# Kernel tuning notes

Hardware: AMD Instinct MI355X
Metric: run time of the kernel (lower is better)

Reference implementation:

```python
import jax, jax.numpy as jnp
import numpy as np

N = 100000   # nodes
E = 640000   # edges
D = 128      # in_channels
C = 40       # out_channels (classes)


def setup_inputs() -> dict:
    key = jax.random.key(0)
    ks = jax.random.split(key, 6)
    x = jax.random.normal(ks[0], (N, D), jnp.float32)
    edge_index = jax.random.randint(ks[1], (2, E), 0, N)
    edge_weight = jax.random.uniform(ks[2], (E,), jnp.float32)
    # 8 block convs (4 blocks x 2) stacked, + final conv
    Wb = jax.random.normal(ks[3], (8, D, D), jnp.float32) / np.sqrt(D)
    bb = jnp.zeros((8, D), jnp.float32)
    Wf = jax.random.normal(ks[4], (D, C), jnp.float32) / np.sqrt(D)
    bf = jnp.zeros((C,), jnp.float32)
    return dict(x=x, edge_index=edge_index, edge_weight=edge_weight,
                Wb=Wb, bb=bb, Wf=Wf, bf=bf)


def _gcn(x, W, b, src, dst, w):
    """PyG GCNConv (normalize=True) with self-loops already appended to src/dst/w."""
    n = x.shape[0]
    h = x @ W                                   # [N, out]
    deg = jax.ops.segment_sum(w, dst, num_segments=n)
    dinv = jnp.where(deg > 0, jax.lax.rsqrt(deg), 0.0)
    norm = dinv[src] * w * dinv[dst]            # [E+N]
    out = jax.ops.segment_sum(h[src] * norm[:, None], dst, num_segments=n)
    return out + b


def reference(x, edge_index, edge_weight, Wb, bb, Wf, bf):
    n = x.shape[0]
    loop = jnp.arange(n)
    src = jnp.concatenate([edge_index[0], loop])
    dst = jnp.concatenate([edge_index[1], loop])
    w = jnp.concatenate([edge_weight, jnp.ones((n,), x.dtype)])
    # forward only runs blocks 1-4 (blocks 5-7 unused in the original forward)
    for i in range(4):
        identity = x
        x = jax.nn.relu(_gcn(x, Wb[2 * i], bb[2 * i], src, dst, w))
        # dropout: identity in eval mode
        x = jax.nn.relu(_gcn(x, Wb[2 * i + 1], bb[2 * i + 1], src, dst, w))
        # F.normalize: row-wise L2 with eps=1e-12
        x = x / jnp.maximum(jnp.linalg.norm(x, axis=1, keepdims=True), 1e-12)
        x = (x + identity) / 2
    x = _gcn(x, Wf, bf, src, dst, w)
    return jax.nn.log_softmax(x, axis=1)
```

## Files before the change

### kernel.cpp

```cpp
#include <hip/hip_runtime.h>
#include <math.h>

#define NN 100000
#define EE 640000
#define DD 128
#define CC 40
#define FIXS 4194304.0f

typedef __bf16 bf16x8 __attribute__((ext_vector_type(8)));
typedef float f32x4 __attribute__((ext_vector_type(4)));
typedef unsigned short us8 __attribute__((ext_vector_type(8)));

__device__ inline unsigned short f2b(float f) {
    union { float f; unsigned u; } v; v.f = f;
    unsigned u = v.u;
    return (unsigned short)((u + 0x7FFFu + ((u >> 16) & 1u)) >> 16);
}
__device__ inline float b2f(unsigned short b) {
    union { unsigned u; float f; } v; v.u = ((unsigned)b) << 16;
    return v.f;
}


__global__ __launch_bounds__(256) void k_edge1(const int* __restrict__ dst,
                                               const float* __restrict__ w,
                                               unsigned long long* __restrict__ degcnt,
                                               int* __restrict__ pos) {
    int e = blockIdx.x * 256 + threadIdx.x;
    if (e < EE) {
        int d = dst[e];
        unsigned long long pk =
            ((unsigned long long)(unsigned)(w[e] * FIXS) << 32) | 1ull;
        unsigned long long old = atomicAdd(&degcnt[d], pk);
        pos[e] = (int)(old & 0xffffffffull);
    }
}

__global__ __launch_bounds__(256) void k_scan1(const unsigned long long* __restrict__ degcnt,
                                               float* __restrict__ dinv,
                                               int* __restrict__ out,
                                               int* __restrict__ partial) {
    __shared__ int lds[256];
    int t = threadIdx.x;
    int base = blockIdx.x * 1024 + t * 4;
    int v[4]; int s = 0;
    #pragma unroll
    for (int j = 0; j < 4; ++j) {
        int idx = base + j;
        unsigned long long dc = (idx < NN) ? degcnt[idx] : 0ull;
        v[j] = (int)(dc & 0xffffffffull);
        s += v[j];
        if (idx < NN)
            dinv[idx] = rsqrtf((float)(unsigned)(dc >> 32) * (1.0f / FIXS) + 1.0f);
    }
    lds[t] = s;
    __syncthreads();
    for (int off = 1; off < 256; off <<= 1) {
        int x = lds[t];
        int y = (t >= off) ? lds[t - off] : 0;
        __syncthreads();
        lds[t] = x + y;
        __syncthreads();
    }
    int excl = lds[t] - s;
    if (t == 255) partial[blockIdx.x] = lds[255];
    int run = excl;
    #pragma unroll
    for (int j = 0; j < 4; ++j) {
        int idx = base + j;
        if (idx < NN) out[idx] = run;
        run += v[j];
    }
}

__global__ __launch_bounds__(128) void k_scan2(int* __restrict__ partial) {
    __shared__ int lds[128];
    int t = threadIdx.x;
    int v = (t < 98) ? partial[t] : 0;
    lds[t] = v;
    __syncthreads();
    for (int off = 1; off < 128; off <<= 1) {
        int x = lds[t];
        int y = (t >= off) ? lds[t - off] : 0;
        __syncthreads();
        lds[t] = x + y;
        __syncthreads();
    }
    if (t < 98) partial[t] = lds[t] - v;
}

__global__ __launch_bounds__(256) void k_scan3(int* __restrict__ rp,
                                               const int* __restrict__ partial) {
    int i = blockIdx.x * 256 + threadIdx.x;
    if (i < NN) rp[i] += partial[i >> 10];
    if (i == 0) rp[NN] = EE;
}

__global__ __launch_bounds__(256) void k_scatter(const int* __restrict__ src,
                                                 const int* __restrict__ dst,
                                                 const float* __restrict__ w,
                                                 const float* __restrict__ dinv,
                                                 const int* __restrict__ rp,
                                                 const int* __restrict__ pos,
                                                 int* __restrict__ col,
                                                 float* __restrict__ val) {
    int e = blockIdx.x * 256 + threadIdx.x;
    if (e < EE) {
        int s = src[e], d = dst[e];
        int p = rp[d] + pos[e];
        col[p] = s;
        val[p] = dinv[s] * w[e] * dinv[d];
    }
}


__global__ __launch_bounds__(256) void k_prep_w(const float* __restrict__ Wb,
                                                unsigned short* __restrict__ WT) {
    int idx = blockIdx.x * 256 + threadIdx.x;
    if (idx >= 8 * DD * DD) return;
    int m = idx >> 14;
    int n = (idx >> 7) & 127;
    int k = idx & 127;
    WT[idx] = f2b(Wb[(size_t)m * DD * DD + (size_t)k * DD + n]);
}

__global__ __launch_bounds__(256) void k_prep_wf(const float* __restrict__ Wf,
                                                 unsigned short* __restrict__ WfT) {
    int idx = blockIdx.x * 256 + threadIdx.x;
    if (idx >= 48 * DD) return;
    int n = idx >> 7;
    int k = idx & 127;
    WfT[idx] = (n < CC) ? f2b(Wf[(size_t)k * CC + n]) : 0;
}

__global__ __launch_bounds__(256) void k_x2bf(const float* __restrict__ x,
                                              float* __restrict__ A,
                                              unsigned short* __restrict__ Abf) {
    int idx = blockIdx.x * 256 + threadIdx.x;
    if (idx >= NN * DD / 4) return;
    float4 v = ((const float4*)x)[idx];
    ((float4*)A)[idx] = v;
    ushort4 r;
    r.x = f2b(v.x); r.y = f2b(v.y); r.z = f2b(v.z); r.w = f2b(v.w);
    ((ushort4*)Abf)[idx] = r;
}

__global__ __launch_bounds__(256) void k_mm_mfma(const unsigned short* __restrict__ X,
                                                 const unsigned short* __restrict__ WT,
                                                 unsigned short* __restrict__ H) {
    int wid = threadIdx.x >> 6;
    int lane = threadIdx.x & 63;
    int r0 = blockIdx.x * 64 + wid * 16;
    int sl = lane & 15, g = lane >> 4;
    int arow = r0 + sl;
    if (arow >= NN) arow = NN - 1;

    f32x4 acc[8];
    #pragma unroll
    for (int n = 0; n < 8; ++n) acc[n] = (f32x4){0.f, 0.f, 0.f, 0.f};

    const bf16x8* xrow = (const bf16x8*)(X + (size_t)arow * DD);
    #pragma unroll
    for (int kc = 0; kc < 4; ++kc) {
        bf16x8 a = xrow[kc * 4 + g];
        #pragma unroll
        for (int n = 0; n < 8; ++n) {
            const bf16x8* wrow = (const bf16x8*)(WT + (size_t)(n * 16 + sl) * DD);
            bf16x8 b = wrow[kc * 4 + g];
            acc[n] = __builtin_amdgcn_mfma_f32_16x16x32_bf16(a, b, acc[n], 0, 0, 0);
        }
    }
    #pragma unroll
    for (int n = 0; n < 8; ++n) {
        #pragma unroll
        for (int v = 0; v < 4; ++v) {
            int row = r0 + g * 4 + v;
            if (row < NN) H[(size_t)row * DD + n * 16 + sl] = f2b(acc[n][v]);
        }
    }
}

__global__ __launch_bounds__(256) void k_mm_final(const unsigned short* __restrict__ X,
                                                  const unsigned short* __restrict__ WfT,
                                                  const float* __restrict__ bf_,
                                                  float* __restrict__ out) {
    int wid = threadIdx.x >> 6;
    int lane = threadIdx.x & 63;
    int r0 = blockIdx.x * 64 + wid * 16;
    int sl = lane & 15, g = lane >> 4;
    int arow = r0 + sl;
    if (arow >= NN) arow = NN - 1;

    f32x4 acc[3];
    #pragma unroll
    for (int n = 0; n < 3; ++n) acc[n] = (f32x4){0.f, 0.f, 0.f, 0.f};

    const bf16x8* xrow = (const bf16x8*)(X + (size_t)arow * DD);
    #pragma unroll
    for (int kc = 0; kc < 4; ++kc) {
        bf16x8 a = xrow[kc * 4 + g];
        #pragma unroll
        for (int n = 0; n < 3; ++n) {
            const bf16x8* wrow = (const bf16x8*)(WfT + (size_t)(n * 16 + sl) * DD);
            bf16x8 b = wrow[kc * 4 + g];
            acc[n] = __builtin_amdgcn_mfma_f32_16x16x32_bf16(a, b, acc[n], 0, 0, 0);
        }
    }
    #pragma unroll
    for (int v = 0; v < 4; ++v) {
        int row = r0 + g * 4 + v;
        float vv[3];
        #pragma unroll
        for (int n = 0; n < 3; ++n) {
            int c = n * 16 + sl;
            vv[n] = (c < CC) ? acc[n][v] + bf_[c] : -3.0e38f;
        }
        float m = fmaxf(fmaxf(vv[0], vv[1]), vv[2]);
        m = fmaxf(m, __shfl_xor(m, 1));
        m = fmaxf(m, __shfl_xor(m, 2));
        m = fmaxf(m, __shfl_xor(m, 4));
        m = fmaxf(m, __shfl_xor(m, 8));
        float s = 0.f;
        #pragma unroll
        for (int n = 0; n < 3; ++n)
            s += (n * 16 + sl < CC) ? expf(vv[n] - m) : 0.f;
        s += __shfl_xor(s, 1);
        s += __shfl_xor(s, 2);
        s += __shfl_xor(s, 4);
        s += __shfl_xor(s, 8);
        float ls = logf(s);
        #pragma unroll
        for (int n = 0; n < 3; ++n) {
            int c = n * 16 + sl;
            if (row < NN && c < CC) out[(size_t)row * CC + c] = vv[n] - m - ls;
        }
    }
}


#define AGG_CORE(h_, node_, sl_, a_)                                        \
    {                                                                       \
        float dv = dinv[node_];                                             \
        float dv2 = dv * dv;                                                \
        us8 m_ = ((const us8*)(h_ + (size_t)node_ * DD))[sl_];              \
        _Pragma("unroll")                                                   \
        for (int j = 0; j < 8; ++j) a_[j] = dv2 * b2f(m_[j]);               \
        int e = rp[node_], end = rp[node_ + 1];                             \
        for (; e + 4 <= end; e += 4) {                                      \
            int s0 = col[e], s1 = col[e + 1], s2 = col[e + 2], s3 = col[e + 3]; \
            float v0 = val[e], v1 = val[e + 1], v2 = val[e + 2], v3 = val[e + 3]; \
            us8 q0 = ((const us8*)(h_ + (size_t)s0 * DD))[sl_];             \
            us8 q1 = ((const us8*)(h_ + (size_t)s1 * DD))[sl_];             \
            us8 q2 = ((const us8*)(h_ + (size_t)s2 * DD))[sl_];             \
            us8 q3 = ((const us8*)(h_ + (size_t)s3 * DD))[sl_];             \
            _Pragma("unroll")                                               \
            for (int j = 0; j < 8; ++j)                                     \
                a_[j] += (v0 * b2f(q0[j]) + v1 * b2f(q1[j]))                \
                       + (v2 * b2f(q2[j]) + v3 * b2f(q3[j]));               \
        }                                                                   \
        for (; e < end; ++e) {                                              \
            int s0 = col[e];                                                \
            float v0 = val[e];                                              \
            us8 q0 = ((const us8*)(h_ + (size_t)s0 * DD))[sl_];             \
            _Pragma("unroll")                                               \
            for (int j = 0; j < 8; ++j) a_[j] += v0 * b2f(q0[j]);           \
        }                                                                   \
    }

__global__ __launch_bounds__(256) void k_agg128(const unsigned short* __restrict__ h,
                                                const float* __restrict__ dinv,
                                                const int* __restrict__ rp,
                                                const int* __restrict__ col,
                                                const float* __restrict__ val,
                                                const float* __restrict__ bias,
                                                unsigned short* __restrict__ outb) {
    int node = blockIdx.x * 16 + (threadIdx.x >> 4);
    int sl = threadIdx.x & 15;
    if (node >= NN) return;
    float a[8];
    AGG_CORE(h, node, sl, a);
    float4 bz0 = ((const float4*)bias)[sl * 2];
    float4 bz1 = ((const float4*)bias)[sl * 2 + 1];
    float bb[8] = {bz0.x, bz0.y, bz0.z, bz0.w, bz1.x, bz1.y, bz1.z, bz1.w};
    us8 r;
    #pragma unroll
    for (int j = 0; j < 8; ++j) r[j] = f2b(fmaxf(a[j] + bb[j], 0.f));
    ((us8*)(outb + (size_t)node * DD))[sl] = r;
}

__global__ __launch_bounds__(256) void k_agg128_nr(const unsigned short* __restrict__ h,
                                                   const float* __restrict__ dinv,
                                                   const int* __restrict__ rp,
                                                   const int* __restrict__ col,
                                                   const float* __restrict__ val,
                                                   const float* __restrict__ bias,
                                                   float* __restrict__ A,
                                                   unsigned short* __restrict__ Abf) {
    int node = blockIdx.x * 16 + (threadIdx.x >> 4);
    int sl = threadIdx.x & 15;
    if (node >= NN) return;
    float a[8];
    AGG_CORE(h, node, sl, a);
    float4 bz0 = ((const float4*)bias)[sl * 2];
    float4 bz1 = ((const float4*)bias)[sl * 2 + 1];
    float bb[8] = {bz0.x, bz0.y, bz0.z, bz0.w, bz1.x, bz1.y, bz1.z, bz1.w};
    float ss = 0.f;
    #pragma unroll
    for (int j = 0; j < 8; ++j) {
        a[j] = fmaxf(a[j] + bb[j], 0.f);
        ss += a[j] * a[j];
    }
    ss += __shfl_xor(ss, 1);
    ss += __shfl_xor(ss, 2);
    ss += __shfl_xor(ss, 4);
    ss += __shfl_xor(ss, 8);
    float sc = 1.0f / fmaxf(sqrtf(ss), 1e-12f);
    float4 a0 = ((const float4*)(A + (size_t)node * DD))[sl * 2];
    float4 a1 = ((const float4*)(A + (size_t)node * DD))[sl * 2 + 1];
    float av[8] = {a0.x, a0.y, a0.z, a0.w, a1.x, a1.y, a1.z, a1.w};
    us8 rb;
    #pragma unroll
    for (int j = 0; j < 8; ++j) {
        av[j] = (a[j] * sc + av[j]) * 0.5f;
        rb[j] = f2b(av[j]);
    }
    float4 o0 = {av[0], av[1], av[2], av[3]};
    float4 o1 = {av[4], av[5], av[6], av[7]};
    ((float4*)(A + (size_t)node * DD))[sl * 2] = o0;
    ((float4*)(A + (size_t)node * DD))[sl * 2 + 1] = o1;
    ((us8*)(Abf + (size_t)node * DD))[sl] = rb;
}

__global__ __launch_bounds__(256) void k_agg_plain(const unsigned short* __restrict__ h,
                                                   const float* __restrict__ dinv,
                                                   const int* __restrict__ rp,
                                                   const int* __restrict__ col,
                                                   const float* __restrict__ val,
                                                   unsigned short* __restrict__ outb) {
    int node = blockIdx.x * 16 + (threadIdx.x >> 4);
    int sl = threadIdx.x & 15;
    if (node >= NN) return;
    float a[8];
    AGG_CORE(h, node, sl, a);
    us8 r;
    #pragma unroll
    for (int j = 0; j < 8; ++j) r[j] = f2b(a[j]);
    ((us8*)(outb + (size_t)node * DD))[sl] = r;
}


extern "C" void kernel_launch(void* const* d_in, const int* in_sizes, int n_in,
                              void* d_out, int out_size, void* d_ws, size_t ws_size,
                              hipStream_t stream) {
    const float* x  = (const float*)d_in[0];
    const int*   ei = (const int*)d_in[1];
    const float* ew = (const float*)d_in[2];
    const float* Wb = (const float*)d_in[3];
    const float* bb = (const float*)d_in[4];
    const float* Wf = (const float*)d_in[5];
    const float* bf_ = (const float*)d_in[6];
    const int* src = ei;
    const int* dst = ei + EE;
    float* out = (float*)d_out;

    char* p = (char*)d_ws;
    float*              A      = (float*)p;              p += (size_t)NN * DD * 4;
    unsigned short*     Abf    = (unsigned short*)p;     p += (size_t)NN * DD * 2;
    unsigned short*     Bbf    = (unsigned short*)p;     p += (size_t)NN * DD * 2;
    unsigned short*     Cbf    = (unsigned short*)p;     p += (size_t)NN * DD * 2;
    unsigned short*     Gbf    = (unsigned short*)p;     p += (size_t)NN * DD * 2;
    unsigned short*     WT     = (unsigned short*)p;     p += (size_t)8 * DD * DD * 2;
    unsigned short*     WfT    = (unsigned short*)p;     p += (size_t)48 * DD * 2;
    unsigned long long* degcnt = (unsigned long long*)p; p += (size_t)NN * 8;
    float* dinv = (float*)p; p += (size_t)NN * 4;
    int*   rp   = (int*)p;   p += (size_t)(NN + 1) * 4;
    int*   pos  = (int*)p;   p += (size_t)EE * 4;
    int*   col  = (int*)p;   p += (size_t)EE * 4;
    float* val  = (float*)p; p += (size_t)EE * 4;
    int*   partial = (int*)p; p += 128 * 4;

    hipMemsetAsync(degcnt, 0, (size_t)NN * 8, stream);

    k_edge1<<<(EE + 255) / 256, 256, 0, stream>>>(dst, ew, degcnt, pos);
    k_scan1<<<98, 256, 0, stream>>>(degcnt, dinv, rp, partial);
    k_scan2<<<1, 128, 0, stream>>>(partial);
    k_scan3<<<(NN + 255) / 256, 256, 0, stream>>>(rp, partial);
    k_scatter<<<(EE + 255) / 256, 256, 0, stream>>>(src, dst, ew, dinv, rp, pos, col, val);

    k_prep_w<<<(8 * DD * DD + 255) / 256, 256, 0, stream>>>(Wb, WT);
    k_prep_wf<<<(48 * DD + 255) / 256, 256, 0, stream>>>(Wf, WfT);
    k_x2bf<<<(NN * DD / 4 + 255) / 256, 256, 0, stream>>>(x, A, Abf);

    for (int blk = 0; blk < 4; ++blk) {
        k_mm_mfma<<<(NN + 63) / 64, 256, 0, stream>>>(Abf, WT + (size_t)(2 * blk) * DD * DD, Bbf);
        k_agg128<<<(NN + 15) / 16, 256, 0, stream>>>(Bbf, dinv, rp, col, val, bb + (size_t)(2 * blk) * DD, Cbf);
        k_mm_mfma<<<(NN + 63) / 64, 256, 0, stream>>>(Cbf, WT + (size_t)(2 * blk + 1) * DD * DD, Bbf);
        k_agg128_nr<<<(NN + 15) / 16, 256, 0, stream>>>(Bbf, dinv, rp, col, val, bb + (size_t)(2 * blk + 1) * DD, A, Abf);
    }
    k_agg_plain<<<(NN + 15) / 16, 256, 0, stream>>>(Abf, dinv, rp, col, val, Gbf);
    k_mm_final<<<(NN + 63) / 64, 256, 0, stream>>>(Gbf, WfT, bf_, out);
}
```

Baseline: 725.0 us.

## Reorder final GCN to matmul-then-aggregate and drop fp32 residual copy

The final layer now projects to 40 (padded to 64) classes before aggregation, so the last sparse gather reads 64-wide bf16 rows instead of 128-wide. Bias and log_softmax are fused into the new aggregation kernel. The fp32 residual buffer is removed, and the residual now comes from the bf16 activations. This cuts memory traffic but adds extra bf16 rounding on the residual path, which may affect accuracy.

```diff
diff --git a/kernel.cpp b/kernel.cpp
--- a/kernel.cpp
+++ b/kernel.cpp
@@ -127,19 +127,17 @@
 __global__ __launch_bounds__(256) void k_prep_wf(const float* __restrict__ Wf,
                                                  unsigned short* __restrict__ WfT) {
     int idx = blockIdx.x * 256 + threadIdx.x;
-    if (idx >= 48 * DD) return;
+    if (idx >= 64 * DD) return;
     int n = idx >> 7;
     int k = idx & 127;
     WfT[idx] = (n < CC) ? f2b(Wf[(size_t)k * CC + n]) : 0;
 }
 
 __global__ __launch_bounds__(256) void k_x2bf(const float* __restrict__ x,
-                                              float* __restrict__ A,
                                               unsigned short* __restrict__ Abf) {
     int idx = blockIdx.x * 256 + threadIdx.x;
     if (idx >= NN * DD / 4) return;
     float4 v = ((const float4*)x)[idx];
-    ((float4*)A)[idx] = v;
     ushort4 r;
     r.x = f2b(v.x); r.y = f2b(v.y); r.z = f2b(v.z); r.w = f2b(v.w);
     ((ushort4*)Abf)[idx] = r;
@@ -180,10 +178,9 @@
     }
 }
 
-__global__ __launch_bounds__(256) void k_mm_final(const unsigned short* __restrict__ X,
-                                                  const unsigned short* __restrict__ WfT,
-                                                  const float* __restrict__ bf_,
-                                                  float* __restrict__ out) {
+__global__ __launch_bounds__(256) void k_mm40b(const unsigned short* __restrict__ X,
+                                               const unsigned short* __restrict__ WfT,
+                                               unsigned short* __restrict__ H) {
     int wid = threadIdx.x >> 6;
     int lane = threadIdx.x & 63;
     int r0 = blockIdx.x * 64 + wid * 16;
@@ -191,68 +188,47 @@
     int arow = r0 + sl;
     if (arow >= NN) arow = NN - 1;
 
-    f32x4 acc[3];
-    #pragma unroll
-    for (int n = 0; n < 3; ++n) acc[n] = (f32x4){0.f, 0.f, 0.f, 0.f};
+    f32x4 acc[4];
+    #pragma unroll
+    for (int n = 0; n < 4; ++n) acc[n] = (f32x4){0.f, 0.f, 0.f, 0.f};
 
     const bf16x8* xrow = (const bf16x8*)(X + (size_t)arow * DD);
     #pragma unroll
     for (int kc = 0; kc < 4; ++kc) {
         bf16x8 a = xrow[kc * 4 + g];
         #pragma unroll
-        for (int n = 0; n < 3; ++n) {
+        for (int n = 0; n < 4; ++n) {
             const bf16x8* wrow = (const bf16x8*)(WfT + (size_t)(n * 16 + sl) * DD);
             bf16x8 b = wrow[kc * 4 + g];
             acc[n] = __builtin_amdgcn_mfma_f32_16x16x32_bf16(a, b, acc[n], 0, 0, 0);
         }
     }
     #pragma unroll
-    for (int v = 0; v < 4; ++v) {
-        int row = r0 + g * 4 + v;
-        float vv[3];
-        #pragma unroll
-        for (int n = 0; n < 3; ++n) {
-            int c = n * 16 + sl;
-            vv[n] = (c < CC) ? acc[n][v] + bf_[c] : -3.0e38f;
+    for (int n = 0; n < 4; ++n) {
+        #pragma unroll
+        for (int v = 0; v < 4; ++v) {
+            int row = r0 + g * 4 + v;
+            if (row < NN) H[(size_t)row * 64 + n * 16 + sl] = f2b(acc[n][v]);
         }
-        float m = fmaxf(fmaxf(vv[0], vv[1]), vv[2]);
-        m = fmaxf(m, __shfl_xor(m, 1));
-        m = fmaxf(m, __shfl_xor(m, 2));
-        m = fmaxf(m, __shfl_xor(m, 4));
-        m = fmaxf(m, __shfl_xor(m, 8));
-        float s = 0.f;
-        #pragma unroll
-        for (int n = 0; n < 3; ++n)
-            s += (n * 16 + sl < CC) ? expf(vv[n] - m) : 0.f;
-        s += __shfl_xor(s, 1);
-        s += __shfl_xor(s, 2);
-        s += __shfl_xor(s, 4);
-        s += __shfl_xor(s, 8);
-        float ls = logf(s);
-        #pragma unroll
-        for (int n = 0; n < 3; ++n) {
-            int c = n * 16 + sl;
-            if (row < NN && c < CC) out[(size_t)row * CC + c] = vv[n] - m - ls;
-        }
-    }
-}
-
-
-#define AGG_CORE(h_, node_, sl_, a_)                                        \
+    }
+}
+
+
+#define AGG_CORE(h_, node_, sl_, a_, STRIDE_)                               \
     {                                                                       \
         float dv = dinv[node_];                                             \
         float dv2 = dv * dv;                                                \
-        us8 m_ = ((const us8*)(h_ + (size_t)node_ * DD))[sl_];              \
+        us8 m_ = ((const us8*)(h_ + (size_t)node_ * STRIDE_))[sl_];         \
         _Pragma("unroll")                                                   \
         for (int j = 0; j < 8; ++j) a_[j] = dv2 * b2f(m_[j]);               \
         int e = rp[node_], end = rp[node_ + 1];                             \
         for (; e + 4 <= end; e += 4) {                                      \
             int s0 = col[e], s1 = col[e + 1], s2 = col[e + 2], s3 = col[e + 3]; \
             float v0 = val[e], v1 = val[e + 1], v2 = val[e + 2], v3 = val[e + 3]; \
-            us8 q0 = ((const us8*)(h_ + (size_t)s0 * DD))[sl_];             \
-            us8 q1 = ((const us8*)(h_ + (size_t)s1 * DD))[sl_];             \
-            us8 q2 = ((const us8*)(h_ + (size_t)s2 * DD))[sl_];             \
-            us8 q3 = ((const us8*)(h_ + (size_t)s3 * DD))[sl_];             \
+            us8 q0 = ((const us8*)(h_ + (size_t)s0 * STRIDE_))[sl_];        \
+            us8 q1 = ((const us8*)(h_ + (size_t)s1 * STRIDE_))[sl_];        \
+            us8 q2 = ((const us8*)(h_ + (size_t)s2 * STRIDE_))[sl_];        \
+            us8 q3 = ((const us8*)(h_ + (size_t)s3 * STRIDE_))[sl_];        \
             _Pragma("unroll")                                               \
             for (int j = 0; j < 8; ++j)                                     \
                 a_[j] += (v0 * b2f(q0[j]) + v1 * b2f(q1[j]))                \
@@ -261,7 +237,7 @@
         for (; e < end; ++e) {                                              \
             int s0 = col[e];                                                \
             float v0 = val[e];                                              \
-            us8 q0 = ((const us8*)(h_ + (size_t)s0 * DD))[sl_];             \
+            us8 q0 = ((const us8*)(h_ + (size_t)s0 * STRIDE_))[sl_];        \
             _Pragma("unroll")                                               \
             for (int j = 0; j < 8; ++j) a_[j] += v0 * b2f(q0[j]);           \
         }                                                                   \
@@ -278,7 +254,7 @@
     int sl = threadIdx.x & 15;
     if (node >= NN) return;
     float a[8];
-    AGG_CORE(h, node, sl, a);
+    AGG_CORE(h, node, sl, a, DD);
     float4 bz0 = ((const float4*)bias)[sl * 2];
     float4 bz1 = ((const float4*)bias)[sl * 2 + 1];
     float bb[8] = {bz0.x, bz0.y, bz0.z, bz0.w, bz1.x, bz1.y, bz1.z, bz1.w};
@@ -294,13 +270,12 @@
                                                    const int* __restrict__ col,
                                                    const float* __restrict__ val,
                                                    const float* __restrict__ bias,
-                                                   float* __restrict__ A,
                                                    unsigned short* __restrict__ Abf) {
     int node = blockIdx.x * 16 + (threadIdx.x >> 4);
     int sl = threadIdx.x & 15;
     if (node >= NN) return;
     float a[8];
-    AGG_CORE(h, node, sl, a);
+    AGG_CORE(h, node, sl, a, DD);
     float4 bz0 = ((const float4*)bias)[sl * 2];
     float4 bz1 = ((const float4*)bias)[sl * 2 + 1];
     float bb[8] = {bz0.x, bz0.y, bz0.z, bz0.w, bz1.x, bz1.y, bz1.z, bz1.w};
@@ -315,37 +290,60 @@
     ss += __shfl_xor(ss, 4);
     ss += __shfl_xor(ss, 8);
     float sc = 1.0f / fmaxf(sqrtf(ss), 1e-12f);
-    float4 a0 = ((const float4*)(A + (size_t)node * DD))[sl * 2];
-    float4 a1 = ((const float4*)(A + (size_t)node * DD))[sl * 2 + 1];
-    float av[8] = {a0.x, a0.y, a0.z, a0.w, a1.x, a1.y, a1.z, a1.w};
+    us8 oldb = ((const us8*)(Abf + (size_t)node * DD))[sl];
     us8 rb;
     #pragma unroll
-    for (int j = 0; j < 8; ++j) {
-        av[j] = (a[j] * sc + av[j]) * 0.5f;
-        rb[j] = f2b(av[j]);
-    }
-    float4 o0 = {av[0], av[1], av[2], av[3]};
-    float4 o1 = {av[4], av[5], av[6], av[7]};
-    ((float4*)(A + (size_t)node * DD))[sl * 2] = o0;
-    ((float4*)(A + (size_t)node * DD))[sl * 2 + 1] = o1;
+    for (int j = 0; j < 8; ++j)
+        rb[j] = f2b((a[j] * sc + b2f(oldb[j])) * 0.5f);
     ((us8*)(Abf + (size_t)node * DD))[sl] = rb;
 }
 
-__global__ __launch_bounds__(256) void k_agg_plain(const unsigned short* __restrict__ h,
+__global__ __launch_bounds__(256) void k_agg_final(const unsigned short* __restrict__ h,
                                                    const float* __restrict__ dinv,
                                                    const int* __restrict__ rp,
                                                    const int* __restrict__ col,
                                                    const float* __restrict__ val,
-                                                   unsigned short* __restrict__ outb) {
-    int node = blockIdx.x * 16 + (threadIdx.x >> 4);
-    int sl = threadIdx.x & 15;
+                                                   const float* __restrict__ bias,
+                                                   float* __restrict__ out) {
+    int node = blockIdx.x * 32 + (threadIdx.x >> 3);
+    int sl = threadIdx.x & 7;
     if (node >= NN) return;
     float a[8];
-    AGG_CORE(h, node, sl, a);
-    us8 r;
-    #pragma unroll
-    for (int j = 0; j < 8; ++j) r[j] = f2b(a[j]);
-    ((us8*)(outb + (size_t)node * DD))[sl] = r;
+    AGG_CORE(h, node, sl, a, 64);
+    bool real = sl < 5;
+    float vv[8];
+    if (real) {
+        float4 bz0 = ((const float4*)bias)[sl * 2];
+        float4 bz1 = ((const float4*)bias)[sl * 2 + 1];
+        float bb[8] = {bz0.x, bz0.y, bz0.z, bz0.w, bz1.x, bz1.y, bz1.z, bz1.w};
+        #pragma unroll
+        for (int j = 0; j < 8; ++j) vv[j] = a[j] + bb[j];
+    } else {
+        #pragma unroll
+        for (int j = 0; j < 8; ++j) vv[j] = -3.0e38f;
+    }
+    float m = vv[0];
+    #pragma unroll
+    for (int j = 1; j < 8; ++j) m = fmaxf(m, vv[j]);
+    m = fmaxf(m, __shfl_xor(m, 1));
+    m = fmaxf(m, __shfl_xor(m, 2));
+    m = fmaxf(m, __shfl_xor(m, 4));
+    float s = 0.f;
+    if (real) {
+        #pragma unroll
+        for (int j = 0; j < 8; ++j) s += expf(vv[j] - m);
+    }
+    s += __shfl_xor(s, 1);
+    s += __shfl_xor(s, 2);
+    s += __shfl_xor(s, 4);
+    float ls = m + logf(s);
+    if (real) {
+        float4 o0 = {vv[0] - ls, vv[1] - ls, vv[2] - ls, vv[3] - ls};
+        float4 o1 = {vv[4] - ls, vv[5] - ls, vv[6] - ls, vv[7] - ls};
+        float* orow = out + (size_t)node * CC + sl * 8;
+        *(float4*)(orow) = o0;
+        *(float4*)(orow + 4) = o1;
+    }
 }
 
 
@@ -364,13 +362,12 @@
     float* out = (float*)d_out;
 
     char* p = (char*)d_ws;
-    float*              A      = (float*)p;              p += (size_t)NN * DD * 4;
     unsigned short*     Abf    = (unsigned short*)p;     p += (size_t)NN * DD * 2;
     unsigned short*     Bbf    = (unsigned short*)p;     p += (size_t)NN * DD * 2;
     unsigned short*     Cbf    = (unsigned short*)p;     p += (size_t)NN * DD * 2;
-    unsigned short*     Gbf    = (unsigned short*)p;     p += (size_t)NN * DD * 2;
+    unsigned short*     H48    = (unsigned short*)p;     p += (size_t)NN * 64 * 2;
     unsigned short*     WT     = (unsigned short*)p;     p += (size_t)8 * DD * DD * 2;
-    unsigned short*     WfT    = (unsigned short*)p;     p += (size_t)48 * DD * 2;
+    unsigned short*     WfT    = (unsigned short*)p;     p += (size_t)64 * DD * 2;
     unsigned long long* degcnt = (unsigned long long*)p; p += (size_t)NN * 8;
     float* dinv = (float*)p; p += (size_t)NN * 4;
     int*   rp   = (int*)p;   p += (size_t)(NN + 1) * 4;
@@ -388,15 +385,15 @@
     k_scatter<<<(EE + 255) / 256, 256, 0, stream>>>(src, dst, ew, dinv, rp, pos, col, val);
 
     k_prep_w<<<(8 * DD * DD + 255) / 256, 256, 0, stream>>>(Wb, WT);
-    k_prep_wf<<<(48 * DD + 255) / 256, 256, 0, stream>>>(Wf, WfT);
-    k_x2bf<<<(NN * DD / 4 + 255) / 256, 256, 0, stream>>>(x, A, Abf);
+    k_prep_wf<<<(64 * DD + 255) / 256, 256, 0, stream>>>(Wf, WfT);
+    k_x2bf<<<(NN * DD / 4 + 255) / 256, 256, 0, stream>>>(x, Abf);
 
     for (int blk = 0; blk < 4; ++blk) {
         k_mm_mfma<<<(NN + 63) / 64, 256, 0, stream>>>(Abf, WT + (size_t)(2 * blk) * DD * DD, Bbf);
         k_agg128<<<(NN + 15) / 16, 256, 0, stream>>>(Bbf, dinv, rp, col, val, bb + (size_t)(2 * blk) * DD, Cbf);
         k_mm_mfma<<<(NN + 63) / 64, 256, 0, stream>>>(Cbf, WT + (size_t)(2 * blk + 1) * DD * DD, Bbf);
-        k_agg128_nr<<<(NN + 15) / 16, 256, 0, stream>>>(Bbf, dinv, rp, col, val, bb + (size_t)(2 * blk + 1) * DD, A, Abf);
-    }
-    k_agg_plain<<<(NN + 15) / 16, 256, 0, stream>>>(Abf, dinv, rp, col, val, Gbf);
-    k_mm_final<<<(NN + 63) / 64, 256, 0, stream>>>(Gbf, WfT, bf_, out);
-}
+        k_agg128_nr<<<(NN + 15) / 16, 256, 0, stream>>>(Bbf, dinv, rp, col, val, bb + (size_t)(2 * blk + 1) * DD, Abf);
+    }
+    k_mm40b<<<(NN + 63) / 64, 256, 0, stream>>>(Abf, WfT, H48);
+    k_agg_final<<<(NN + 31) / 32, 256, 0, stream>>>(H48, dinv, rp, col, val, bf_, out);
+}
```

New measurement: 666.0 us. -8.1%, faster.
